# Optimization experiments

Measured on AMD Instinct MI355X. Metric: run time of the kernel, lower is better.

## Reference

```python
import jax, jax.numpy as jnp
import numpy as np

B, C, H, W = 16, 256, 64, 64
OUT_C = 3
N_TOKENS = 512
N_RES = 3
RED = 4
CB = C // RED  # bottleneck channels in ResChain
DN = ('NCHW', 'OIHW', 'NCHW')


def _conv(x, w, pad):
    return jax.lax.conv_general_dilated(x, w, (1, 1), pad, dimension_numbers=DN)


def setup_inputs() -> dict:
    key = jax.random.key(0)
    ks = jax.random.split(key, 8)
    return {
        'input': jax.random.normal(ks[0], (B, C, H, W), jnp.float32),
        'embed': jax.random.normal(ks[1], (C, N_TOKENS), jnp.float32),  # Quantize codebook [dim, n_embed]
        'res_w1': jax.random.normal(ks[2], (N_RES, CB, C, 3, 3), jnp.float32) * 0.02,
        'res_b1': jnp.zeros((N_RES, CB), jnp.float32),
        'res_w2': jax.random.normal(ks[3], (N_RES, C, CB, 1, 1), jnp.float32) * 0.02,
        'res_b2': jnp.zeros((N_RES, C), jnp.float32),
        'out_w': jax.random.normal(ks[4], (OUT_C, C, 1, 1), jnp.float32) * 0.02,
        'out_b': jnp.zeros((OUT_C,), jnp.float32),
    }


def reference(input, embed, res_w1, res_b1, res_w2, res_b2, out_w, out_b):
    sg = jax.lax.stop_gradient
    # --- Quantize (VQ-VAE codebook lookup, straight-through) ---
    x = jnp.transpose(input, (0, 2, 3, 1))  # [B,H,W,C]
    flat = x.reshape(-1, C)                  # [N, C]
    # squared L2 distance to each code: ||f||^2 - 2 f.e + ||e||^2
    dist = (flat * flat).sum(-1, keepdims=True) - 2.0 * (flat @ embed) + (embed * embed).sum(0)
    idx = jnp.argmin(dist, axis=-1).reshape(B, H, W)        # [B,H,W] int
    quantize = jnp.take(embed.T, idx, axis=0)               # embed_code: [B,H,W,C]
    diff = jnp.mean((sg(quantize) - x) ** 2)
    quantize = x + sg(quantize - x)                         # straight-through
    q = jnp.transpose(quantize, (0, 3, 1, 2))               # [B,C,H,W]
    # --- dec: ResChain(n_res_block) + 1x1 conv ---
    for i in range(N_RES):
        h = jax.nn.relu(q)
        h = _conv(h, res_w1[i], 'SAME') + res_b1[i][None, :, None, None]
        h = jax.nn.relu(h)
        h = _conv(h, res_w2[i], 'VALID') + res_b2[i][None, :, None, None]
        q = q + h
    quant = _conv(q, out_w, 'VALID') + out_b[None, :, None, None]  # [B,OUT_C,H,W]
    # --- wordfreq: per-batch bincount over idx (no grad) ---
    flat_idx = idx.reshape(B, -1)
    seg = (flat_idx + jnp.arange(B, dtype=flat_idx.dtype)[:, None] * N_TOKENS).reshape(-1)
    counts = jax.ops.segment_sum(jnp.ones_like(seg, jnp.float32), seg, num_segments=B * N_TOKENS)
    wordfreq = counts.reshape(B, N_TOKENS) / float(H * W)
    return quant, diff.reshape(1), wordfreq
```

## Files before the change

### kernel.cpp

```cpp
#include <hip/hip_runtime.h>


typedef __attribute__((ext_vector_type(8))) short short8;
typedef __attribute__((ext_vector_type(16))) float f32x16;
typedef __attribute__((ext_vector_type(8))) _Float16 half8;
typedef __attribute__((ext_vector_type(2))) _Float16 half2_t;
typedef unsigned short ushort_t;
typedef unsigned long long u64;

#define WS_QA    0
#define WS_QB    8388608
#define WS_ET    16777216
#define WS_EN    16842752
#define WS_EPK   16843264
#define WS_W1PK  16908800
#define WS_W2PK  17129984
#define WS_DIFF  17154560
#define WS_TOK   17154568
#define WS_DST   17220104
#define WS_FN    17285640
#define WS_WL    17351176
#define WS_LUT   17416720

#define MARGIN 0.12f

__device__ inline ushort_t f2bf(float f) {
  unsigned u = __float_as_uint(f);
  return (ushort_t)((u + 0x7fffu + ((u >> 16) & 1u)) >> 16);
}
__device__ inline float bf2f(ushort_t h) { return __uint_as_float(((unsigned)h) << 16); }
union HU { _Float16 h; ushort_t u; };
union S8H { short8 s; half8 h; half2_t h2[4]; };

__global__ __launch_bounds__(256) void prep_kernel(
    const float* __restrict__ embed, const float* __restrict__ w1,
    const float* __restrict__ w2, float* __restrict__ ws, float* __restrict__ wf) {
  int i = blockIdx.x * 256 + threadIdx.x;
  if (i < 131072) {
    int t = i >> 8, c = i & 255;
    ((ushort_t*)(ws + WS_ET))[i] = f2bf(embed[c * 512 + t]);
  }
  if (i < 512) {
    float s = 0.f;
    for (int c = 0; c < 256; ++c) { float v = embed[c * 512 + i]; s += v * v; }
    ws[WS_EN + i] = s;
  }
  if (i < 131072) {
    int j = i & 7, lane = (i >> 3) & 63, at = (i >> 9) & 15, ks = i >> 13;
    int code = at * 32 + (lane & 31);
    int c = ks * 16 + (lane >> 5) * 8 + j;
    HU cv; cv.h = (_Float16)embed[c * 512 + code];
    ((ushort_t*)(ws + WS_EPK))[i] = cv.u;
  }
  if (i < 442368) {
    int j = i & 7; int lane = (i >> 3) & 63; int of = (i >> 9) & 1;
    int k16 = (i >> 10) & 15; int rest = i >> 14;
    int tap = rest % 9; int layer = rest / 9;
    int oc = of * 32 + (lane & 31);
    int c = k16 * 16 + (lane >> 5) * 8 + j;
    ((ushort_t*)(ws + WS_W1PK))[i] = f2bf(w1[((layer * 64 + oc) * 256 + c) * 9 + tap]);
  }
  if (i < 49152) {
    int j = i & 7, lane = (i >> 3) & 63, at = (i >> 9) & 7, ks = (i >> 12) & 3, l = i >> 14;
    int co = at * 32 + (lane & 31), cb = ks * 16 + (lane >> 5) * 8 + j;
    ((ushort_t*)(ws + WS_W2PK))[i] = f2bf(w2[(l * 256 + co) * 64 + cb]);
  }
  if (i < 8192) wf[i] = 0.f;
  if (i == 0) { ws[WS_DIFF] = 0.f; ((int*)(ws + WS_WL))[0] = 0; }
}

__global__ __launch_bounds__(256) void lut_kernel(
    const float* __restrict__ embed, const float* __restrict__ w1,
    float* __restrict__ lut) {
  int g = blockIdx.x * 256 + threadIdx.x;
  int t = g & 511, oc = g >> 9;
  float acc[9];
#pragma unroll
  for (int tap = 0; tap < 9; ++tap) acc[tap] = 0.f;
#pragma unroll 4
  for (int c = 0; c < 256; ++c) {
    float v = fmaxf(bf2f(f2bf(embed[c * 512 + t])), 0.f);
    const float* wr = w1 + (size_t)(oc * 256 + c) * 9;
#pragma unroll
    for (int tap = 0; tap < 9; ++tap) acc[tap] += v * wr[tap];
  }
#pragma unroll
  for (int tap = 0; tap < 9; ++tap)
    lut[((size_t)t * 9 + tap) * 64 + oc] = acc[tap];
}

__global__ __launch_bounds__(512, 4) void dist_kernel(
    const float* __restrict__ input, const half8* __restrict__ epk,
    const float* __restrict__ enorm, int* __restrict__ tok,
    float* __restrict__ dst, float* __restrict__ fnv, int* __restrict__ wl) {
  __shared__ __align__(16) ushort_t sfp[2048 * 8];
  __shared__ float senorm[512];
  __shared__ float trim1[512], trim2[512];
  __shared__ int   trii[512];

  int blk = blockIdx.x, b = blk >> 6, hw0 = (blk & 63) << 6;
  int tid = threadIdx.x, lane = tid & 63, wave = tid >> 6;
  senorm[tid] = enorm[tid];

  {
    int cg = tid >> 3, sub = tid & 7;
    int ks_s = cg >> 2, hi_s = (cg >> 1) & 1, jq = cg & 1;
    const float* src0 = input + ((size_t)(b * 256 + cg * 4)) * 4096 + hw0 + sub * 8;
    float vv[4][8];
#pragma unroll
    for (int m = 0; m < 4; ++m) {
      const float4* s4 = (const float4*)(src0 + (size_t)m * 4096);
      float4 aa = s4[0], bb = s4[1];
      vv[m][0] = aa.x; vv[m][1] = aa.y; vv[m][2] = aa.z; vv[m][3] = aa.w;
      vv[m][4] = bb.x; vv[m][5] = bb.y; vv[m][6] = bb.z; vv[m][7] = bb.w;
    }
    u64* sfp64 = (u64*)sfp;
#pragma unroll
    for (int i = 0; i < 8; ++i) {
      int pl = sub * 8 + i;
      int bt = pl >> 5, lw = (pl & 31) + 32 * hi_s;
      u64 pk = 0;
#pragma unroll
      for (int m = 0; m < 4; ++m) {
        HU cv; cv.h = (_Float16)vv[m][i];
        pk |= ((u64)cv.u) << (16 * m);
      }
      sfp64[((bt * 16 + ks_s) * 64 + lw) * 2 + jq] = pk;
    }
  }
  __syncthreads();

  f32x16 acc[2][2];
#pragma unroll
  for (int bt = 0; bt < 2; ++bt)
#pragma unroll
    for (int a = 0; a < 2; ++a)
#pragma unroll
      for (int r = 0; r < 16; ++r) acc[bt][a][r] = 0.f;

  const short8* sfp8 = (const short8*)sfp;
  float fnp0 = 0.f, fnp1 = 0.f;
#pragma unroll 2
  for (int ks = 0; ks < 16; ++ks) {
    S8H u0, u1;
    u0.s = sfp8[ks * 64 + lane];
    u1.s = sfp8[(16 + ks) * 64 + lane];
#if __has_builtin(__builtin_amdgcn_fdot2)
#pragma unroll
    for (int k = 0; k < 4; ++k) {
      fnp0 = __builtin_amdgcn_fdot2(u0.h2[k], u0.h2[k], fnp0, false);
      fnp1 = __builtin_amdgcn_fdot2(u1.h2[k], u1.h2[k], fnp1, false);
    }
#else
#pragma unroll
    for (int k = 0; k < 8; ++k) {
      float v0 = (float)u0.h[k], v1 = (float)u1.h[k];
      fnp0 += v0 * v0; fnp1 += v1 * v1;
    }
#endif
#pragma unroll
    for (int a = 0; a < 2; ++a) {
      half8 ah = epk[(ks * 16 + wave * 2 + a) * 64 + lane];
      acc[0][a] = __builtin_amdgcn_mfma_f32_32x32x16_f16(ah, u0.h, acc[0][a], 0, 0, 0);
      acc[1][a] = __builtin_amdgcn_mfma_f32_32x32x16_f16(ah, u1.h, acc[1][a], 0, 0, 0);
    }
  }
  fnp0 += __shfl_xor(fnp0, 32, 64);
  fnp1 += __shfl_xor(fnp1, 32, 64);

  int hi5 = lane >> 5;
#pragma unroll
  for (int bt = 0; bt < 2; ++bt) {
    float m1 = 3.4e38f, m2 = 3.4e38f; int i1 = 0;
#pragma unroll
    for (int a = 0; a < 2; ++a)
#pragma unroll
      for (int r = 0; r < 16; ++r) {
        int code = (wave * 2 + a) * 32 + (r & 3) + 8 * (r >> 2) + 4 * hi5;
        float v = senorm[code] - 2.0f * acc[bt][a][r];
        if (v < m1) { m2 = m1; m1 = v; i1 = code; }
        else if (v < m2) m2 = v;
      }
    float o1 = __shfl_xor(m1, 32, 64);
    float o2 = __shfl_xor(m2, 32, 64);
    int   oi = __shfl_xor(i1, 32, 64);
    float n2 = fminf(fmaxf(m1, o1), fminf(m2, o2));
    float n1 = fminf(m1, o1);
    int   ni = (o1 < m1) ? oi : i1;
    if (lane < 32) {
      int p = bt * 32 + lane;
      trim1[p * 8 + wave] = n1; trim2[p * 8 + wave] = n2; trii[p * 8 + wave] = ni;
    }
  }
  __syncthreads();

  if (wave == 0) {
    int p = lane;
    float m1 = trim1[p * 8], m2 = trim2[p * 8]; int i1 = trii[p * 8];
#pragma unroll
    for (int w = 1; w < 8; ++w) {
      float a1 = trim1[p * 8 + w], a2 = trim2[p * 8 + w]; int ai = trii[p * 8 + w];
      float n2 = fminf(fmaxf(m1, a1), fminf(m2, a2));
      if (a1 < m1) { m1 = a1; i1 = ai; }
      m2 = n2;
    }
    float myfn = (lane < 32) ? fnp0 : fnp1;
    int gpos = blk * 64 + p;
    tok[gpos] = i1;
    dst[gpos] = myfn + m1;
    fnv[gpos] = myfn;
    bool flag = (m2 - m1 < MARGIN);
    u64 mk = __ballot(flag);
    int base = 0;
    if (lane == 0 && mk) base = atomicAdd(wl, (int)__popcll(mk));
    base = __shfl(base, 0, 64);
    if (flag) {
      int off = (int)__popcll(mk & ((1ull << lane) - 1ull));
      wl[1 + base + off] = gpos;
    }
  }
}

__global__ __launch_bounds__(256) void redo_kernel(
    const float* __restrict__ input, const float* __restrict__ embed,
    const float* __restrict__ enorm, const int* __restrict__ wl,
    int* __restrict__ tok, float* __restrict__ dst, const float* __restrict__ fnv) {
  __shared__ float sf[256], rv[256];
  __shared__ int   ri[256];
  int n = wl[0];
  int tid = threadIdx.x;
  for (int e = blockIdx.x; e < n; e += gridDim.x) {
    int gpos = wl[1 + e];
    int b = gpos >> 12, hw = gpos & 4095;
    sf[tid] = input[((size_t)(b * 256 + tid)) * 4096 + hw];
    __syncthreads();
    float d0 = 0.f, d1 = 0.f;
#pragma unroll 4
    for (int c = 0; c < 256; ++c) {
      float fv = sf[c];
      d0 += fv * embed[c * 512 + tid];
      d1 += fv * embed[c * 512 + 256 + tid];
    }
    float v0 = enorm[tid] - 2.f * d0;
    float v1 = enorm[256 + tid] - 2.f * d1;
    float bv; int bi;
    if (v1 < v0) { bv = v1; bi = 256 + tid; } else { bv = v0; bi = tid; }
    rv[tid] = bv; ri[tid] = bi;
    __syncthreads();
    for (int s = 128; s > 0; s >>= 1) {
      if (tid < s) {
        float ov = rv[tid + s]; int oi2 = ri[tid + s];
        if (ov < rv[tid] || (ov == rv[tid] && oi2 < ri[tid])) { rv[tid] = ov; ri[tid] = oi2; }
      }
      __syncthreads();
    }
    if (tid == 0) { tok[gpos] = ri[0]; dst[gpos] = fnv[gpos] + rv[0]; }
    __syncthreads();
  }
}

__global__ __launch_bounds__(256) void finalize_kernel(
    const int* __restrict__ tok, const float* __restrict__ dst,
    const ushort_t* __restrict__ embedT, float* __restrict__ wf,
    float* __restrict__ diffp, ushort_t* __restrict__ qout) {
  int blk = blockIdx.x;
  int tid = threadIdx.x, lane = tid & 63, wave = tid >> 6;
  int gbase = blk * 64;
  int b = gbase >> 12;
  if (wave == 0) {
    int t = tok[gbase + lane];
    atomicAdd(&wf[b * 512 + t], 1.0f / 4096.0f);
    float d = dst[gbase + lane];
#pragma unroll
    for (int off = 32; off >= 1; off >>= 1) d += __shfl_down(d, off, 64);
    if (lane == 0) atomicAdd(diffp, d);
  }
#pragma unroll 1
  for (int j = 0; j < 16; ++j) {
    int p = wave * 16 + j;
    int t = __builtin_amdgcn_readfirstlane(tok[gbase + p]);
    const u64* src = (const u64*)(embedT + (size_t)t * 256);
    u64* dstp = (u64*)(qout + ((size_t)(gbase + p)) * 256);
    dstp[lane] = src[lane];
  }
}

__global__ __launch_bounds__(512, 4) void layer0_kernel(
    const ushort_t* __restrict__ qin, ushort_t* __restrict__ qout,
    const int* __restrict__ tok, const float* __restrict__ lut,
    const float* __restrict__ b1, const ushort_t* __restrict__ w2pk,
    const float* __restrict__ b2) {
  __shared__ __align__(16) char arena[28672];
  ushort_t* hbuf   = (ushort_t*)arena;
  float*    sb2    = (float*)(arena + 9728);
  int*      stok   = (int*)(arena + 10752);
  ushort_t* qstage = (ushort_t*)(arena + 11264);

  int blk = blockIdx.x;
  int b = blk >> 6; int t = blk & 63;
  int ty0 = (t >> 3) << 3;
  int tx0 = (t & 7) << 3;
  int tid = threadIdx.x, lane = tid & 63, w = tid >> 6;
  int l31 = lane & 31, kb5 = lane >> 5;

  if (tid < 256) sb2[tid] = b2[tid];
  if (tid < 100) {
    int yy = tid / 10, xx = tid - yy * 10;
    int sy = ty0 + yy - 1, sx = tx0 + xx - 1;
    stok[tid] = (sy >= 0 && sy < 64 && sx >= 0 && sx < 64)
              ? tok[b * 4096 + sy * 64 + sx] : -1;
  }
  __syncthreads();

  {
    int px = tid >> 3, oc8 = tid & 7;
    int y = px >> 3, x = px & 7;
    float a[8];
    const float* bp = b1 + oc8 * 8;
#pragma unroll
    for (int j = 0; j < 8; ++j) a[j] = bp[j];
#pragma unroll
    for (int dy = 0; dy < 3; ++dy)
#pragma unroll
      for (int dx = 0; dx < 3; ++dx) {
        int tt = stok[(y + dy) * 10 + (x + dx)];
        if (tt >= 0) {
          const float4* r = (const float4*)(lut + ((size_t)tt * 9 + dy * 3 + dx) * 64 + oc8 * 8);
          float4 v0 = r[0], v1 = r[1];
          a[0] += v0.x; a[1] += v0.y; a[2] += v0.z; a[3] += v0.w;
          a[4] += v1.x; a[5] += v1.y; a[6] += v1.z; a[7] += v1.w;
        }
      }
    u64 p0 = 0, p1 = 0;
#pragma unroll
    for (int j = 0; j < 4; ++j) p0 |= ((u64)f2bf(fmaxf(a[j], 0.f))) << (16 * j);
#pragma unroll
    for (int j = 0; j < 4; ++j) p1 |= ((u64)f2bf(fmaxf(a[4 + j], 0.f))) << (16 * j);
    *(u64*)(hbuf + px * 76 + oc8 * 8) = p0;
    *(u64*)(hbuf + px * 76 + oc8 * 8 + 4) = p1;
  }
  __syncthreads();

  const short8* w2p = (const short8*)w2pk;
  int pt2 = w & 1, coq = w >> 1;
#pragma unroll 1
  for (int ch = 0; ch < 2; ++ch) {
    short8 qv[2];
#pragma unroll
    for (int it = 0; it < 2; ++it) {
      int u = it * 512 + tid;
      int p = u >> 4, c8 = u & 15;
      int gy = ty0 + (p >> 3), gx = tx0 + (p & 7);
      qv[it] = *(const short8*)(qin + ((size_t)(b * 4096 + gy * 64 + gx)) * 256 + ch * 128 + c8 * 8);
    }

    f32x16 acc2;
#pragma unroll
    for (int r = 0; r < 16; ++r) acc2[r] = 0.f;
#pragma unroll
    for (int ks = 0; ks < 4; ++ks) {
      short8 A = *(const short8*)(hbuf + (pt2 * 32 + l31) * 76 + ks * 16 + kb5 * 8);
      short8 B = w2p[(ks * 8 + ch * 4 + coq) * 64 + lane];
      acc2 = __builtin_amdgcn_mfma_f32_32x32x16_bf16(A, B, acc2, 0, 0, 0);
    }
    {
      int cc = coq * 32 + l31;
      float bb2 = sb2[ch * 128 + cc];
#pragma unroll
      for (int r = 0; r < 16; ++r) {
        int row = (r & 3) + 8 * (r >> 2) + 4 * kb5;
        qstage[(pt2 * 32 + row) * 136 + cc] = f2bf(acc2[r] + bb2);
      }
    }
    __syncthreads();
#pragma unroll
    for (int it = 0; it < 2; ++it) {
      int u = it * 512 + tid;
      int p = u >> 4, c8 = u & 15;
      short8 hv = *(const short8*)(qstage + p * 136 + c8 * 8);
      int gy = ty0 + (p >> 3), gx = tx0 + (p & 7);
      size_t gidx = ((size_t)(b * 4096 + gy * 64 + gx)) * 256 + ch * 128 + c8 * 8;
      short8 ov;
#pragma unroll
      for (int k2 = 0; k2 < 8; ++k2)
        ov[k2] = (short)f2bf(bf2f((ushort_t)qv[it][k2]) + bf2f((ushort_t)hv[k2]));
      *(short8*)(qout + gidx) = ov;
    }
    __syncthreads();
  }
}

__global__ __launch_bounds__(512, 4) void fused_layer(
    const ushort_t* __restrict__ qin, ushort_t* __restrict__ qout,
    const ushort_t* __restrict__ w1pk, const float* __restrict__ b1,
    const ushort_t* __restrict__ w2pk, const float* __restrict__ b2, int l) {
  __shared__ __align__(16) char arena[38912];
  ushort_t* hbuf   = (ushort_t*)arena;
  float*    sb2    = (float*)(arena + 9728);
  short8*   stg    = (short8*)(arena + 10752);
  float*    red    = (float*)(arena + 10752);
  ushort_t* qstage = (ushort_t*)(arena + 10752);

  int blk = blockIdx.x;
  int b = blk >> 6; int t = blk & 63;
  int ty0 = (t >> 3) << 3;
  int tx0 = (t & 7) << 3;
  int tid = threadIdx.x, lane = tid & 63, w = tid >> 6;
  int pt = w & 1, ot = (w >> 1) & 1, kh = w >> 2;
  int l31 = lane & 31, kb5 = lane >> 5;

  if (tid < 256) sb2[tid] = b2[l * 256 + tid];

  const short8* wp  = (const short8*)w1pk + (size_t)l * 18432;
  const short8* w2p = (const short8*)w2pk;

  short8 sreg[2];
  auto loadch = [&](int cs) {
#pragma unroll
    for (int s = 0; s < 2; ++s) {
      int u = s * 512 + tid;
      if (u < 800) {
        int cg = u & 7; int pix = u >> 3; int y = pix / 10; int x = pix - y * 10;
        int sy = ty0 + y - 1, sx = tx0 + x - 1;
        if (sy >= 0 && sy < 64 && sx >= 0 && sx < 64) {
          sreg[s] = *(const short8*)(qin + ((size_t)(b * 4096 + sy * 64 + sx)) * 256 + cs * 64 + cg * 8);
        } else {
          short8 z;
#pragma unroll
          for (int k2 = 0; k2 < 8; ++k2) z[k2] = 0;
          sreg[s] = z;
        }
      }
    }
  };
  auto writech = [&](int buf) {
#pragma unroll
    for (int s = 0; s < 2; ++s) {
      int u = s * 512 + tid;
      if (u < 800) {
        int cg = u & 7; int pix = u >> 3; int y = pix / 10; int x = pix - y * 10;
        short8 sv = sreg[s];
#pragma unroll
        for (int k2 = 0; k2 < 8; ++k2) if (sv[k2] < 0) sv[k2] = 0;
        stg[buf * 880 + (y * 8 + cg) * 11 + x] = sv;
      }
    }
  };

  f32x16 acc;
#pragma unroll
  for (int r = 0; r < 16; ++r) acc[r] = 0.f;

  int py0 = pt * 4 + (l31 >> 3);
  int px0 = lane & 7;

  loadch(0);
  writech(0);
#pragma unroll 1
  for (int cs = 0; cs < 4; ++cs) {
    __syncthreads();
    if (cs < 3) loadch(cs + 1);
    int buf = cs & 1;
#pragma unroll 1
    for (int dy = 0; dy < 3; ++dy) {
#pragma unroll 1
      for (int dx = 0; dx < 3; ++dx) {
        int tap = dy * 3 + dx;
#pragma unroll
        for (int ks2 = 0; ks2 < 2; ++ks2) {
          int kk = kh * 2 + ks2;
          short8 A = stg[buf * 880 + ((py0 + dy) * 8 + kk * 2 + kb5) * 11 + px0 + dx];
          short8 B = wp[(tap * 16 + cs * 4 + kk) * 128 + ot * 64 + lane];
          acc = __builtin_amdgcn_mfma_f32_32x32x16_bf16(A, B, acc, 0, 0, 0);
        }
      }
    }
    if (cs < 3) writech((cs + 1) & 1);
  }
  __syncthreads();

  if (kh == 1) {
    float4* d = (float4*)(red + (w & 3) * 1024 + lane * 16);
#pragma unroll
    for (int r4 = 0; r4 < 4; ++r4) {
      float4 v; v.x = acc[r4 * 4]; v.y = acc[r4 * 4 + 1];
      v.z = acc[r4 * 4 + 2]; v.w = acc[r4 * 4 + 3];
      d[r4] = v;
    }
  }
  __syncthreads();
  if (kh == 0) {
    const float* s = red + (w & 3) * 1024 + lane * 16;
    int oc = ot * 32 + l31;
    float bb = b1[l * 64 + oc];
#pragma unroll
    for (int r = 0; r < 16; ++r) {
      int row = (r & 3) + 8 * (r >> 2) + 4 * kb5;
      hbuf[(pt * 32 + row) * 76 + oc] = f2bf(fmaxf(acc[r] + s[r] + bb, 0.f));
    }
  }
  __syncthreads();

  int pt2 = w & 1, coq = w >> 1;
#pragma unroll 1
  for (int ch = 0; ch < 2; ++ch) {
    short8 qv[2];
#pragma unroll
    for (int it = 0; it < 2; ++it) {
      int u = it * 512 + tid;
      int p = u >> 4, c8 = u & 15;
      int gy = ty0 + (p >> 3), gx = tx0 + (p & 7);
      qv[it] = *(const short8*)(qin + ((size_t)(b * 4096 + gy * 64 + gx)) * 256 + ch * 128 + c8 * 8);
    }

    f32x16 acc2;
#pragma unroll
    for (int r = 0; r < 16; ++r) acc2[r] = 0.f;
#pragma unroll
    for (int ks = 0; ks < 4; ++ks) {
      short8 A = *(const short8*)(hbuf + (pt2 * 32 + l31) * 76 + ks * 16 + kb5 * 8);
      short8 B = w2p[((l * 4 + ks) * 8 + ch * 4 + coq) * 64 + lane];
      acc2 = __builtin_amdgcn_mfma_f32_32x32x16_bf16(A, B, acc2, 0, 0, 0);
    }
    {
      int cc = coq * 32 + l31;
      float bb2 = sb2[ch * 128 + cc];
#pragma unroll
      for (int r = 0; r < 16; ++r) {
        int row = (r & 3) + 8 * (r >> 2) + 4 * kb5;
        qstage[(pt2 * 32 + row) * 136 + cc] = f2bf(acc2[r] + bb2);
      }
    }
    __syncthreads();
#pragma unroll
    for (int it = 0; it < 2; ++it) {
      int u = it * 512 + tid;
      int p = u >> 4, c8 = u & 15;
      short8 hv = *(const short8*)(qstage + p * 136 + c8 * 8);
      int gy = ty0 + (p >> 3), gx = tx0 + (p & 7);
      size_t gidx = ((size_t)(b * 4096 + gy * 64 + gx)) * 256 + ch * 128 + c8 * 8;
      short8 ov;
#pragma unroll
      for (int k2 = 0; k2 < 8; ++k2)
        ov[k2] = (short)f2bf(bf2f((ushort_t)qv[it][k2]) + bf2f((ushort_t)hv[k2]));
      *(short8*)(qout + gidx) = ov;
    }
    __syncthreads();
  }
}

__global__ __launch_bounds__(256) void final_kernel(
    const ushort_t* __restrict__ qbuf, const float* __restrict__ ow,
    const float* __restrict__ ob, float* __restrict__ out,
    const float* __restrict__ ws) {
  int t = blockIdx.x * 256 + threadIdx.x;
  int pos = t >> 4, c16 = t & 15;
  const ushort_t* qp = qbuf + (size_t)pos * 256 + c16 * 16;
  short8 v0 = *(const short8*)qp;
  short8 v1 = *(const short8*)(qp + 8);
  float a0 = 0.f, a1 = 0.f, a2 = 0.f;
#pragma unroll
  for (int k = 0; k < 16; ++k) {
    float f = bf2f((ushort_t)(k < 8 ? v0[k] : v1[k - 8]));
    int c = c16 * 16 + k;
    a0 += f * ow[c];
    a1 += f * ow[256 + c];
    a2 += f * ow[512 + c];
  }
#pragma unroll
  for (int off = 1; off < 16; off <<= 1) {
    a0 += __shfl_xor(a0, off, 64);
    a1 += __shfl_xor(a1, off, 64);
    a2 += __shfl_xor(a2, off, 64);
  }
  if (c16 == 0) {
    int b = pos >> 12, hw = pos & 4095;
    out[(b * 3 + 0) * 4096 + hw] = a0 + ob[0];
    out[(b * 3 + 1) * 4096 + hw] = a1 + ob[1];
    out[(b * 3 + 2) * 4096 + hw] = a2 + ob[2];
  }
  if (t == 0) out[196608] = ws[WS_DIFF] * (1.0f / 16777216.0f);
}

extern "C" void kernel_launch(void* const* d_in, const int* in_sizes, int n_in,
                              void* d_out, int out_size, void* d_ws, size_t ws_size,
                              hipStream_t stream) {
  (void)in_sizes; (void)n_in; (void)out_size; (void)ws_size;
  const float* input = (const float*)d_in[0];
  const float* embed = (const float*)d_in[1];
  const float* w1 = (const float*)d_in[2];
  const float* b1 = (const float*)d_in[3];
  const float* b2 = (const float*)d_in[5];
  const float* ow = (const float*)d_in[6];
  const float* ob = (const float*)d_in[7];
  float* ws = (float*)d_ws;
  float* out = (float*)d_out;
  float* wf = out + 196609;

  ushort_t* qA = (ushort_t*)(ws + WS_QA);
  ushort_t* qB = (ushort_t*)(ws + WS_QB);
  const ushort_t* et = (const ushort_t*)(ws + WS_ET);
  const half8* epk = (const half8*)(ws + WS_EPK);
  const ushort_t* w1pk = (const ushort_t*)(ws + WS_W1PK);
  const ushort_t* w2pk = (const ushort_t*)(ws + WS_W2PK);
  int*   tok = (int*)(ws + WS_TOK);
  float* dst = ws + WS_DST;
  float* fnv = ws + WS_FN;
  int*   wl  = (int*)(ws + WS_WL);
  float* lut = ws + WS_LUT;

  hipLaunchKernelGGL(prep_kernel, dim3(1728), dim3(256), 0, stream,
                     embed, w1, (const float*)d_in[4], ws, wf);
  hipLaunchKernelGGL(lut_kernel, dim3(128), dim3(256), 0, stream,
                     embed, w1, lut);
  hipLaunchKernelGGL(dist_kernel, dim3(1024), dim3(512), 0, stream,
                     input, epk, ws + WS_EN, tok, dst, fnv, wl);
  hipLaunchKernelGGL(redo_kernel, dim3(1024), dim3(256), 0, stream,
                     input, embed, ws + WS_EN, wl, tok, dst, fnv);
  hipLaunchKernelGGL(finalize_kernel, dim3(1024), dim3(256), 0, stream,
                     tok, dst, et, wf, ws + WS_DIFF, qA);
  hipLaunchKernelGGL(layer0_kernel, dim3(1024), dim3(512), 0, stream,
                     qA, qB, tok, lut, b1, w2pk, b2);
  hipLaunchKernelGGL(fused_layer, dim3(1024), dim3(512), 0, stream,
                     qB, qA, w1pk, b1, w2pk, b2, 1);
  hipLaunchKernelGGL(fused_layer, dim3(1024), dim3(512), 0, stream,
                     qA, qB, w1pk, b1, w2pk, b2, 2);
  hipLaunchKernelGGL(final_kernel, dim3(4096), dim3(256), 0, stream,
                     qB, ow, ob, out, ws);
}
```

Measured before the change: 238.1 us.

## Fuse codebook gather into layer0 conv and drop LUT precompute kernel

Removes the lut_kernel, which precomputed per-token 3x3 conv partial sums, and the materialized quantized tensor written by finalize. Layer 0 now gathers embedding rows by token directly into shared memory and runs the 3x3 conv with MFMA, as the other layers do, and it reads the residual input from the codebook too. Finalize shrinks to the histogram and diff reduction only, and blocks are remapped in the layer kernels for locality. The aim is to cut a kernel launch and a full 16M-element write and read. In exchange, layer 0 does full MFMA conv work instead of cheap LUT adds.

```diff
diff --git a/kernel.cpp b/kernel.cpp
--- a/kernel.cpp
+++ b/kernel.cpp
@@ -20,7 +20,6 @@
 #define WS_DST   17220104
 #define WS_FN    17285640
 #define WS_WL    17351176
-#define WS_LUT   17416720
 
 #define MARGIN 0.12f
 
@@ -67,26 +66,6 @@
   }
   if (i < 8192) wf[i] = 0.f;
   if (i == 0) { ws[WS_DIFF] = 0.f; ((int*)(ws + WS_WL))[0] = 0; }
-}
-
-__global__ __launch_bounds__(256) void lut_kernel(
-    const float* __restrict__ embed, const float* __restrict__ w1,
-    float* __restrict__ lut) {
-  int g = blockIdx.x * 256 + threadIdx.x;
-  int t = g & 511, oc = g >> 9;
-  float acc[9];
-#pragma unroll
-  for (int tap = 0; tap < 9; ++tap) acc[tap] = 0.f;
-#pragma unroll 4
-  for (int c = 0; c < 256; ++c) {
-    float v = fmaxf(bf2f(f2bf(embed[c * 512 + t])), 0.f);
-    const float* wr = w1 + (size_t)(oc * 256 + c) * 9;
-#pragma unroll
-    for (int tap = 0; tap < 9; ++tap) acc[tap] += v * wr[tap];
-  }
-#pragma unroll
-  for (int tap = 0; tap < 9; ++tap)
-    lut[((size_t)t * 9 + tap) * 64 + oc] = acc[tap];
 }
 
 __global__ __launch_bounds__(512, 4) void dist_kernel(
@@ -259,89 +238,143 @@
   }
 }
 
-__global__ __launch_bounds__(256) void finalize_kernel(
+__global__ __launch_bounds__(64) void finalize_kernel(
     const int* __restrict__ tok, const float* __restrict__ dst,
-    const ushort_t* __restrict__ embedT, float* __restrict__ wf,
-    float* __restrict__ diffp, ushort_t* __restrict__ qout) {
-  int blk = blockIdx.x;
-  int tid = threadIdx.x, lane = tid & 63, wave = tid >> 6;
-  int gbase = blk * 64;
+    float* __restrict__ wf, float* __restrict__ diffp) {
+  int gbase = blockIdx.x * 64;
+  int lane = threadIdx.x;
   int b = gbase >> 12;
-  if (wave == 0) {
-    int t = tok[gbase + lane];
-    atomicAdd(&wf[b * 512 + t], 1.0f / 4096.0f);
-    float d = dst[gbase + lane];
-#pragma unroll
-    for (int off = 32; off >= 1; off >>= 1) d += __shfl_down(d, off, 64);
-    if (lane == 0) atomicAdd(diffp, d);
-  }
-#pragma unroll 1
-  for (int j = 0; j < 16; ++j) {
-    int p = wave * 16 + j;
-    int t = __builtin_amdgcn_readfirstlane(tok[gbase + p]);
-    const u64* src = (const u64*)(embedT + (size_t)t * 256);
-    u64* dstp = (u64*)(qout + ((size_t)(gbase + p)) * 256);
-    dstp[lane] = src[lane];
-  }
-}
-
-__global__ __launch_bounds__(512, 4) void layer0_kernel(
-    const ushort_t* __restrict__ qin, ushort_t* __restrict__ qout,
-    const int* __restrict__ tok, const float* __restrict__ lut,
-    const float* __restrict__ b1, const ushort_t* __restrict__ w2pk,
-    const float* __restrict__ b2) {
-  __shared__ __align__(16) char arena[28672];
+  int t = tok[gbase + lane];
+  atomicAdd(&wf[b * 512 + t], 1.0f / 4096.0f);
+  float d = dst[gbase + lane];
+#pragma unroll
+  for (int off = 32; off >= 1; off >>= 1) d += __shfl_down(d, off, 64);
+  if (lane == 0) atomicAdd(diffp, d);
+}
+
+__global__ __launch_bounds__(512, 4) void fused_layer0(
+    const int* __restrict__ tok, const ushort_t* __restrict__ embedT,
+    ushort_t* __restrict__ qout,
+    const ushort_t* __restrict__ w1pk, const float* __restrict__ b1,
+    const ushort_t* __restrict__ w2pk, const float* __restrict__ b2) {
+  __shared__ __align__(16) char arena[38912];
   ushort_t* hbuf   = (ushort_t*)arena;
   float*    sb2    = (float*)(arena + 9728);
-  int*      stok   = (int*)(arena + 10752);
-  ushort_t* qstage = (ushort_t*)(arena + 11264);
-
-  int blk = blockIdx.x;
+  short8*   stg    = (short8*)(arena + 10752);
+  float*    red    = (float*)(arena + 10752);
+  ushort_t* qstage = (ushort_t*)(arena + 10752);
+  __shared__ int stok[100];
+
+  int raw = blockIdx.x;
+  int blk = (raw & 7) * 128 + (raw >> 3);
+
   int b = blk >> 6; int t = blk & 63;
   int ty0 = (t >> 3) << 3;
   int tx0 = (t & 7) << 3;
   int tid = threadIdx.x, lane = tid & 63, w = tid >> 6;
+  int pt = w & 1, ot = (w >> 1) & 1, kh = w >> 2;
   int l31 = lane & 31, kb5 = lane >> 5;
 
   if (tid < 256) sb2[tid] = b2[tid];
-  if (tid < 100) {
-    int yy = tid / 10, xx = tid - yy * 10;
+  if (tid >= 256 && tid < 356) {
+    int u = tid - 256;
+    int yy = u / 10, xx = u - yy * 10;
     int sy = ty0 + yy - 1, sx = tx0 + xx - 1;
-    stok[tid] = (sy >= 0 && sy < 64 && sx >= 0 && sx < 64)
-              ? tok[b * 4096 + sy * 64 + sx] : -1;
-  }
-  __syncthreads();
-
-  {
-    int px = tid >> 3, oc8 = tid & 7;
-    int y = px >> 3, x = px & 7;
-    float a[8];
-    const float* bp = b1 + oc8 * 8;
-#pragma unroll
-    for (int j = 0; j < 8; ++j) a[j] = bp[j];
-#pragma unroll
-    for (int dy = 0; dy < 3; ++dy)
-#pragma unroll
+    stok[u] = (sy >= 0 && sy < 64 && sx >= 0 && sx < 64)
+            ? tok[b * 4096 + sy * 64 + sx] : -1;
+  }
+  __syncthreads();
+
+  const short8* wp  = (const short8*)w1pk;
+  const short8* w2p = (const short8*)w2pk;
+
+  short8 sreg[2];
+  auto loadch = [&](int cs) {
+#pragma unroll
+    for (int s = 0; s < 2; ++s) {
+      int u = s * 512 + tid;
+      if (u < 800) {
+        int cg = u & 7; int pix = u >> 3;
+        int tt = stok[pix];
+        if (tt >= 0) {
+          sreg[s] = *(const short8*)(embedT + (size_t)tt * 256 + cs * 64 + cg * 8);
+        } else {
+          short8 z;
+#pragma unroll
+          for (int k2 = 0; k2 < 8; ++k2) z[k2] = 0;
+          sreg[s] = z;
+        }
+      }
+    }
+  };
+  auto writech = [&](int buf) {
+#pragma unroll
+    for (int s = 0; s < 2; ++s) {
+      int u = s * 512 + tid;
+      if (u < 800) {
+        int cg = u & 7; int pix = u >> 3; int y = pix / 10; int x = pix - y * 10;
+        short8 sv = sreg[s];
+#pragma unroll
+        for (int k2 = 0; k2 < 8; ++k2) if (sv[k2] < 0) sv[k2] = 0;
+        stg[buf * 880 + (y * 8 + cg) * 11 + x] = sv;
+      }
+    }
+  };
+
+  f32x16 acc;
+#pragma unroll
+  for (int r = 0; r < 16; ++r) acc[r] = 0.f;
+
+  int py0 = pt * 4 + (l31 >> 3);
+  int px0 = lane & 7;
+
+  loadch(0);
+  writech(0);
+#pragma unroll 1
+  for (int cs = 0; cs < 4; ++cs) {
+    __syncthreads();
+    if (cs < 3) loadch(cs + 1);
+    int buf = cs & 1;
+#pragma unroll 1
+    for (int dy = 0; dy < 3; ++dy) {
+#pragma unroll 1
       for (int dx = 0; dx < 3; ++dx) {
-        int tt = stok[(y + dy) * 10 + (x + dx)];
-        if (tt >= 0) {
-          const float4* r = (const float4*)(lut + ((size_t)tt * 9 + dy * 3 + dx) * 64 + oc8 * 8);
-          float4 v0 = r[0], v1 = r[1];
-          a[0] += v0.x; a[1] += v0.y; a[2] += v0.z; a[3] += v0.w;
-          a[4] += v1.x; a[5] += v1.y; a[6] += v1.z; a[7] += v1.w;
+        int tap = dy * 3 + dx;
+#pragma unroll
+        for (int ks2 = 0; ks2 < 2; ++ks2) {
+          int kk = kh * 2 + ks2;
+          short8 A = stg[buf * 880 + ((py0 + dy) * 8 + kk * 2 + kb5) * 11 + px0 + dx];
+          short8 B = wp[(tap * 16 + cs * 4 + kk) * 128 + ot * 64 + lane];
+          acc = __builtin_amdgcn_mfma_f32_32x32x16_bf16(A, B, acc, 0, 0, 0);
         }
       }
-    u64 p0 = 0, p1 = 0;
-#pragma unroll
-    for (int j = 0; j < 4; ++j) p0 |= ((u64)f2bf(fmaxf(a[j], 0.f))) << (16 * j);
-#pragma unroll
-    for (int j = 0; j < 4; ++j) p1 |= ((u64)f2bf(fmaxf(a[4 + j], 0.f))) << (16 * j);
-    *(u64*)(hbuf + px * 76 + oc8 * 8) = p0;
-    *(u64*)(hbuf + px * 76 + oc8 * 8 + 4) = p1;
-  }
-  __syncthreads();
-
-  const short8* w2p = (const short8*)w2pk;
+    }
+    if (cs < 3) writech((cs + 1) & 1);
+  }
+  __syncthreads();
+
+  if (kh == 1) {
+    float4* d = (float4*)(red + (w & 3) * 1024 + lane * 16);
+#pragma unroll
+    for (int r4 = 0; r4 < 4; ++r4) {
+      float4 v; v.x = acc[r4 * 4]; v.y = acc[r4 * 4 + 1];
+      v.z = acc[r4 * 4 + 2]; v.w = acc[r4 * 4 + 3];
+      d[r4] = v;
+    }
+  }
+  __syncthreads();
+  if (kh == 0) {
+    const float* s = red + (w & 3) * 1024 + lane * 16;
+    int oc = ot * 32 + l31;
+    float bb = b1[oc];
+#pragma unroll
+    for (int r = 0; r < 16; ++r) {
+      int row = (r & 3) + 8 * (r >> 2) + 4 * kb5;
+      hbuf[(pt * 32 + row) * 76 + oc] = f2bf(fmaxf(acc[r] + s[r] + bb, 0.f));
+    }
+  }
+  __syncthreads();
+
   int pt2 = w & 1, coq = w >> 1;
 #pragma unroll 1
   for (int ch = 0; ch < 2; ++ch) {
@@ -350,8 +383,8 @@
     for (int it = 0; it < 2; ++it) {
       int u = it * 512 + tid;
       int p = u >> 4, c8 = u & 15;
-      int gy = ty0 + (p >> 3), gx = tx0 + (p & 7);
-      qv[it] = *(const short8*)(qin + ((size_t)(b * 4096 + gy * 64 + gx)) * 256 + ch * 128 + c8 * 8);
+      int tt = stok[((p >> 3) + 1) * 10 + (p & 7) + 1];
+      qv[it] = *(const short8*)(embedT + (size_t)tt * 256 + ch * 128 + c8 * 8);
     }
 
     f32x16 acc2;
@@ -401,7 +434,9 @@
   float*    red    = (float*)(arena + 10752);
   ushort_t* qstage = (ushort_t*)(arena + 10752);
 
-  int blk = blockIdx.x;
+  int raw = blockIdx.x;
+  int blk = (raw & 7) * 128 + (raw >> 3);
+
   int b = blk >> 6; int t = blk & 63;
   int ty0 = (t >> 3) << 3;
   int tx0 = (t & 7) << 3;
@@ -588,7 +623,6 @@
   (void)in_sizes; (void)n_in; (void)out_size; (void)ws_size;
   const float* input = (const float*)d_in[0];
   const float* embed = (const float*)d_in[1];
-  const float* w1 = (const float*)d_in[2];
   const float* b1 = (const float*)d_in[3];
   const float* b2 = (const float*)d_in[5];
   const float* ow = (const float*)d_in[6];
@@ -607,20 +641,17 @@
   float* dst = ws + WS_DST;
   float* fnv = ws + WS_FN;
   int*   wl  = (int*)(ws + WS_WL);
-  float* lut = ws + WS_LUT;
 
   hipLaunchKernelGGL(prep_kernel, dim3(1728), dim3(256), 0, stream,
-                     embed, w1, (const float*)d_in[4], ws, wf);
-  hipLaunchKernelGGL(lut_kernel, dim3(128), dim3(256), 0, stream,
-                     embed, w1, lut);
+                     embed, (const float*)d_in[2], (const float*)d_in[4], ws, wf);
   hipLaunchKernelGGL(dist_kernel, dim3(1024), dim3(512), 0, stream,
                      input, epk, ws + WS_EN, tok, dst, fnv, wl);
   hipLaunchKernelGGL(redo_kernel, dim3(1024), dim3(256), 0, stream,
                      input, embed, ws + WS_EN, wl, tok, dst, fnv);
-  hipLaunchKernelGGL(finalize_kernel, dim3(1024), dim3(256), 0, stream,
-                     tok, dst, et, wf, ws + WS_DIFF, qA);
-  hipLaunchKernelGGL(layer0_kernel, dim3(1024), dim3(512), 0, stream,
-                     qA, qB, tok, lut, b1, w2pk, b2);
+  hipLaunchKernelGGL(finalize_kernel, dim3(1024), dim3(64), 0, stream,
+                     tok, dst, wf, ws + WS_DIFF);
+  hipLaunchKernelGGL(fused_layer0, dim3(1024), dim3(512), 0, stream,
+                     tok, et, qB, w1pk, b1, w2pk, b2);
   hipLaunchKernelGGL(fused_layer, dim3(1024), dim3(512), 0, stream,
                      qB, qA, w1pk, b1, w2pk, b2, 1);
   hipLaunchKernelGGL(fused_layer, dim3(1024), dim3(512), 0, stream,
```

Measured after the change: 221.1 us, median of 2. 1.08x faster.
